# Kernel tuning notes

Hardware: AMD Instinct MI355X
Metric: run time of the kernel (lower is better)

The kernel has to match this reference:

```python
import jax, jax.numpy as jnp
import numpy as np

B, S, D, H = 2, 2048, 2048, 16
HD = D // H            # 128
HALF = HD // 2         # 64
SOFTCAP = 50.0
ROPE_BASE = 10000.0


def setup_inputs() -> dict:
    key = jax.random.key(0)
    k1, k2, k3 = jax.random.split(key, 3)
    inputs = jax.random.normal(k1, (B, S, D), dtype=jnp.float32)
    # param init ~ nnx.initializers.normal() (stddev 0.01 default; scale to keep activations sane)
    w_in = jax.random.normal(k2, (D, H, 3 * HD), dtype=jnp.float32) * (1.0 / np.sqrt(D))
    w_out = jax.random.normal(k3, (H, HD, D), dtype=jnp.float32) * (1.0 / np.sqrt(D))
    # RoPE tables: [S, HALF]
    pos = jnp.arange(S, dtype=jnp.float32)[:, None]
    inv_freq = 1.0 / (ROPE_BASE ** (jnp.arange(HALF, dtype=jnp.float32) / HALF))
    ang = pos * inv_freq[None, :]
    rope_sin = jnp.sin(ang)
    rope_cos = jnp.cos(ang)
    # causal mask [1, 1, S, S]
    mask = jnp.tril(jnp.ones((S, S), dtype=bool))[None, None, :, :]
    return {"inputs": inputs, "w_in": w_in, "w_out": w_out,
            "rope_sin": rope_sin, "rope_cos": rope_cos, "mask": mask}


def apply_rope(x, sin, cos):
    # x: [B, S, H, HD]; sin/cos: [S, HALF] -> broadcast [1, S, 1, HALF]
    sin = sin[None, :, None, :]
    cos = cos[None, :, None, :]
    x1, x2 = x[..., :HALF], x[..., HALF:]
    return jnp.concatenate([x1 * cos - x2 * sin, x2 * cos + x1 * sin], axis=-1)


def reference(inputs, w_in, w_out, rope_sin, rope_cos, mask):
    dtype = inputs.dtype
    # fused QKV projection: [B, S, H, 3*HD]
    qkv = jnp.einsum('bsd,bhf->bshf'.replace('bhf', 'dhf'), inputs, w_in)
    q, k, v = jnp.split(qkv, 3, axis=-1)           # each [B, S, H, HD]
    q = apply_rope(q, rope_sin, rope_cos)
    k = apply_rope(k, rope_sin, rope_cos)
    q = q / jnp.sqrt(jnp.asarray(HD, dtype))
    scores = jnp.einsum('bqhd,bkhd->bhqk', q, k)   # [B, H, S, S]
    big_neg = jnp.finfo(dtype).min
    scores = jnp.where(mask, scores, big_neg)
    scores = jnp.tanh(scores / SOFTCAP) * SOFTCAP  # softcap
    attn = jax.nn.softmax(scores, axis=-1)
    x = jnp.einsum('bhqk,bkhd->bqhd', attn, v)     # [B, S, H, HD]
    out = jnp.einsum('bqhd,hdm->bqm', x, w_out)    # [B, S, D]
    return out
```

## Files before the change

kernel.cpp:

```cpp
#include <hip/hip_runtime.h>

#define B_ 2
#define S_ 2048
#define D_ 2048
#define H_ 16
#define HD_ 128
#define NT_ (S_ / 64)

typedef unsigned short u16;
typedef __bf16 bf16x8 __attribute__((ext_vector_type(8)));
typedef float f32x4 __attribute__((ext_vector_type(4)));
typedef u16 u16x8 __attribute__((ext_vector_type(8)));

__device__ __forceinline__ float bf2f(u16 u) {
  unsigned int x = ((unsigned int)u) << 16;
  return __builtin_bit_cast(float, x);
}
__device__ __forceinline__ u16 f2bf(float f) {
  unsigned int u = __builtin_bit_cast(unsigned int, f);
  u += 0x7fffu + ((u >> 16) & 1u);
  return (u16)(u >> 16);
}
__device__ __forceinline__ void async16(const void* g, void* l) {
  __builtin_amdgcn_global_load_lds((const __attribute__((address_space(1))) void*)g,
                                   (__attribute__((address_space(3))) void*)l, 16, 0, 0);
}
__device__ __forceinline__ float vexp2(float x) {
  float r;
  asm("v_exp_f32 %0, %1" : "=v"(r) : "v"(x));
  return r;
}
__device__ __forceinline__ float vrcp(float x) {
  float r;
  asm("v_rcp_f32 %0, %1" : "=v"(r) : "v"(x));
  return r;
}

__global__ __launch_bounds__(256) void conv_f32_bf16(const float* __restrict__ in,
                                                     u16* __restrict__ outp, int n) {
  int idx = (blockIdx.x * 256 + threadIdx.x) * 4;
  int stride = gridDim.x * 256 * 4;
  for (; idx < n; idx += stride) {
    float4 v = *(const float4*)(in + idx);
    ushort4 ov = make_ushort4(f2bf(v.x), f2bf(v.y), f2bf(v.z), f2bf(v.w));
    *(ushort4*)(outp + idx) = ov;
  }
}

__global__ __launch_bounds__(256) void transpose_win(const float* __restrict__ in,
                                                     u16* __restrict__ outp) {
  __shared__ float tile[32][33];
  int n0 = blockIdx.x * 32, k0 = blockIdx.y * 32;
  int tx = threadIdx.x & 31, ty = threadIdx.x >> 5;
  int n = n0 + tx;
  int cc = n >> 7, p = n & 127;
  int q = (p >> 4) & 3;
  int d = ((p >> 6) << 5) + ((q >> 1) << 4) + ((q & 1) << 6) + (p & 15);
  int f = (cc / 3) * 384 + (cc % 3) * 128 + d;
#pragma unroll
  for (int yy = 0; yy < 32; yy += 8)
    tile[ty + yy][tx] = in[(size_t)(k0 + ty + yy) * 6144 + f];
  __syncthreads();
#pragma unroll
  for (int yy = 0; yy < 32; yy += 8)
    outp[(size_t)(n0 + ty + yy) * 2048 + k0 + tx] = f2bf(tile[tx][ty + yy]);
}

__global__ __launch_bounds__(256) void transpose_wout(const float* __restrict__ in,
                                                      u16* __restrict__ outp) {
  __shared__ float tile[32][33];
  int k0 = blockIdx.x * 32, n0 = blockIdx.y * 32;
  int tx = threadIdx.x & 31, ty = threadIdx.x >> 5;
#pragma unroll
  for (int yy = 0; yy < 32; yy += 8) {
    int kk = k0 + ty + yy;
    int hh = kk >> 7, j = kk & 127;
    int hd = (j & 7) * 16 + (j >> 3);
    tile[ty + yy][tx] = in[(size_t)(hh * 128 + hd) * 2048 + n0 + tx];
  }
  __syncthreads();
#pragma unroll
  for (int yy = 0; yy < 32; yy += 8)
    outp[(size_t)(n0 + ty + yy) * 2048 + k0 + tx] = f2bf(tile[tx][ty + yy]);
}

#define BAR __builtin_amdgcn_s_barrier()
#define LGKM0                                          \
  {                                                    \
    asm volatile("s_waitcnt lgkmcnt(0)" ::: "memory"); \
    __builtin_amdgcn_sched_barrier(0);                 \
  }
#define VM3 asm volatile("s_waitcnt vmcnt(3)" ::: "memory")
#define VM4 asm volatile("s_waitcnt vmcnt(4)" ::: "memory")
#define VM0 asm volatile("s_waitcnt vmcnt(0)" ::: "memory")
#define P1 __builtin_amdgcn_s_setprio(1)
#define P0 __builtin_amdgcn_s_setprio(0)

template <int EPI>
__global__ __launch_bounds__(512, 1) void gemm128(
    const u16* __restrict__ A, const u16* __restrict__ Bt, float* __restrict__ C, int K, int N,
    int ntn, u16* __restrict__ Qo, u16* __restrict__ Ko, u16* __restrict__ Vo,
    const float* __restrict__ rsin, const float* __restrict__ rcos) {
  __shared__ alignas(16) u16 lsA[3][128 * 32];
  __shared__ alignas(16) u16 lsB[3][256 * 32];
  const int tid = threadIdx.x;
  const int lane = tid & 63, wid = tid >> 6;
  const int g = lane >> 4, lr = lane & 15;
  const int wm = wid >> 2, wn = wid & 3;

  const int nwg = ntn << 5;
  const int bid = blockIdx.x;
  const int swz = (bid & 7) * (nwg >> 3) + (bid >> 3);
  const int m_idx = swz & 31, n_idx = swz >> 5;
  const size_t m0 = (size_t)m_idx * 128, n0 = (size_t)n_idx * 256;

  const int rowA = tid >> 2, slA = tid & 3;
  const int rowB0 = tid >> 2;
  const int rowB1 = (512 + tid) >> 2;
  const u16* srcA = A + (m0 + rowA) * K + ((slA ^ ((rowA >> 1) & 3)) << 3);
  const u16* srcB0 = Bt + (n0 + rowB0) * K + ((slA ^ ((rowB0 >> 1) & 3)) << 3);
  const u16* srcB1 = Bt + (n0 + rowB1) * K + ((slA ^ ((rowB1 >> 1) & 3)) << 3);

#define STAGE(t, buf)                                         \
  {                                                           \
    const int koff = (t) << 5;                                \
    async16(srcA + koff, (char*)lsA[buf] + tid * 16);         \
    async16(srcB0 + koff, (char*)lsB[buf] + tid * 16);        \
    async16(srcB1 + koff, (char*)lsB[buf] + 8192 + tid * 16); \
  }

  int ofsA[4], ofsB[4];
#pragma unroll
  for (int i = 0; i < 4; ++i) {
    int ra = wm * 64 + i * 16 + lr;
    ofsA[i] = ra * 64 + ((g ^ ((ra >> 1) & 3)) << 4);
    int rb = wn * 64 + i * 16 + lr;
    ofsB[i] = rb * 64 + ((g ^ ((rb >> 1) & 3)) << 4);
  }

  f32x4 acc[4][4] = {};
  const int nk = K >> 5;

  STAGE(0, 0);
  STAGE(1, 1);
  VM3;
  BAR;

#pragma unroll 1
  for (int kt = 0; kt < nk; ++kt) {
    const int tb = kt % 3;
    const int sb = (kt + 2) % 3;
    bf16x8 aF[4], bF[4];
#pragma unroll
    for (int i = 0; i < 4; ++i) aF[i] = *(const bf16x8*)((const char*)lsA[tb] + ofsA[i]);
#pragma unroll
    for (int j = 0; j < 4; ++j) bF[j] = *(const bf16x8*)((const char*)lsB[tb] + ofsB[j]);
    if (kt + 2 < nk) STAGE(kt + 2, sb);
    BAR;
    LGKM0;
    P1;
#pragma unroll
    for (int i = 0; i < 4; ++i)
#pragma unroll
      for (int j = 0; j < 4; ++j)
        acc[i][j] = __builtin_amdgcn_mfma_f32_16x16x32_bf16(aF[i], bF[j], acc[i][j], 0, 0, 0);
    P0;
    if (kt < nk - 2) {
      VM3;
    } else {
      VM0;
    }
    BAR;
  }
#undef STAGE

  if (EPI == 0) {
#pragma unroll
    for (int i = 0; i < 4; ++i)
#pragma unroll
      for (int j = 0; j < 4; ++j)
#pragma unroll
        for (int r = 0; r < 4; ++r) {
          size_t m = m0 + wm * 64 + i * 16 + 4 * g + r;
          size_t n = n0 + wn * 64 + j * 16 + lr;
          C[m * N + n] = acc[i][j][r];
        }
  } else {
    const int c = (int)(n0 >> 7) + (wn >> 1);
    const int h = c / 3, part = c % 3;
    const int wn1 = wn & 1;
    if (part == 2) {
#pragma unroll
      for (int i = 0; i < 4; ++i) {
        int m = (int)m0 + wm * 64 + i * 16 + 4 * g;
        int b = m >> 11, s = m & (S_ - 1);
#pragma unroll
        for (int j = 0; j < 4; ++j) {
          int hd = wn1 * 32 + ((j >> 1) << 4) + ((j & 1) << 6) + lr;
          ushort4 pk;
          pk.x = f2bf(acc[i][j][0]);
          pk.y = f2bf(acc[i][j][1]);
          pk.z = f2bf(acc[i][j][2]);
          pk.w = f2bf(acc[i][j][3]);
          *(ushort4*)(Vo + ((size_t)(b * H_ + h) * HD_ + hd) * S_ + s) = pk;
        }
      }
    } else {
      u16* dstp = (part == 0) ? Qo : Ko;
      const float scl = (part == 0) ? 0.08838834764831845f : 1.0f;
#pragma unroll
      for (int i = 0; i < 4; ++i) {
        int mbase = (int)m0 + wm * 64 + i * 16 + 4 * g;
#pragma unroll
        for (int r = 0; r < 4; ++r) {
          int m = mbase + r;
          int b = m >> 11, s = m & (S_ - 1);
          const float* srow = rsin + s * 64;
          const float* crow = rcos + s * 64;
          u16* op = dstp + ((size_t)(b * H_ + h) * S_ + s) * HD_ + ((wn1 * 16 + lr) << 2);
          ushort4 pk;
          {
            int d = wn1 * 32 + lr;
            float cv = crow[d] * scl, sv = srow[d] * scl;
            float x1 = acc[i][0][r], x2 = acc[i][1][r];
            pk.x = f2bf(x1 * cv - x2 * sv);
            pk.y = f2bf(x2 * cv + x1 * sv);
          }
          {
            int d = wn1 * 32 + 16 + lr;
            float cv = crow[d] * scl, sv = srow[d] * scl;
            float x1 = acc[i][2][r], x2 = acc[i][3][r];
            pk.z = f2bf(x1 * cv - x2 * sv);
            pk.w = f2bf(x2 * cv + x1 * sv);
          }
          *(ushort4*)op = pk;
        }
      }
    }
  }
}

__global__ __launch_bounds__(256) void attn_fwd(const u16* __restrict__ Q, const u16* __restrict__ K,
                                                const u16* __restrict__ VT, u16* __restrict__ X) {
  const int bh = blockIdx.x;
  const int bx = blockIdx.y;
  const int tid = threadIdx.x;
  const int lane = tid & 63, wid = tid >> 6;
  const int g = lane >> 4, lr = lane & 15;

  __shared__ alignas(16) u16 lsK[2][64 * 128];
  __shared__ alignas(16) u16 lsV[2][128 * 64];
  __shared__ alignas(16) u16 lsP[4][16 * 72];

  const u16* Qp = Q + (size_t)bh * S_ * HD_;
  const u16* Kp = K + (size_t)bh * S_ * HD_;
  const u16* Vp = VT + (size_t)bh * HD_ * S_;
  u16* myP = lsP[wid];
  const int b = bh >> 4, h = bh & 15;

  const float c1 = -0.057707802f;
  const float c2 = -144.26950409f;

#define STG_K(t, bufi)                                                  \
  {                                                                     \
    _Pragma("unroll") for (int p = 0; p < 4; ++p) {                     \
      int c = p * 256 + tid;                                            \
      int rowk = c >> 4;                                                \
      int wsk = ((c & 15) << 4) ^ ((rowk & 7) << 4);                    \
      async16((const char*)Kp + (((size_t)((t)*64 + rowk)) << 8) + wsk, \
              (char*)lsK[bufi] + c * 16);                               \
    }                                                                   \
  }
#define STG_V(t, bufi)                                                   \
  {                                                                      \
    _Pragma("unroll") for (int p = 0; p < 4; ++p) {                      \
      int c = p * 256 + tid;                                             \
      int rowv = c >> 3;                                                 \
      int wsv = ((c & 7) << 4) ^ ((rowv & 7) << 4);                      \
      async16((const char*)Vp + (size_t)rowv * (S_ * 2) + (t)*128 + wsv, \
              (char*)lsV[bufi] + c * 16);                                \
    }                                                                    \
  }

#pragma unroll 1
  for (int pass = 0; pass < 2; ++pass) {
    const int qt = pass ? bx : (NT_ - 1 - bx);
    const int qq = qt * 64 + wid * 16 + lr;

    bf16x8 qf[4];
#pragma unroll
    for (int kc = 0; kc < 4; ++kc)
      qf[kc] = *(const bf16x8*)(Qp + (size_t)qq * HD_ + kc * 32 + g * 8);

    f32x4 o[8] = {};
    float psum = 0.f;

    STG_K(0, 0);
    STG_V(0, 0);
    VM0;
    BAR;

    int cur = 0;
    for (int kt = 0; kt <= qt; ++kt) {
      if (kt < qt) STG_K(kt + 1, cur ^ 1);
      f32x4 sc[4];
#pragma unroll
      for (int jn = 0; jn < 4; ++jn) {
        f32x4 a = {0.f, 0.f, 0.f, 0.f};
        const int row = jn * 16 + lr;
        const int sw = (row & 7) << 4;
#pragma unroll
        for (int kc = 0; kc < 4; ++kc) {
          int w = (kc * 64 + g * 16) ^ sw;
          bf16x8 kf = *(const bf16x8*)((const char*)lsK[cur] + row * 256 + w);
          a = __builtin_amdgcn_mfma_f32_16x16x32_bf16(kf, qf[kc], a, 0, 0, 0);
        }
        sc[jn] = a;
      }
#pragma unroll
      for (int jn = 0; jn < 4; ++jn) {
        const int kbase = kt * 64 + jn * 16 + 4 * g;
        float pv[4];
#pragma unroll
        for (int r = 0; r < 4; ++r) {
          float z = vexp2(c1 * sc[jn][r]);
          float p = vexp2(c2 * z * vrcp(1.f + z));
          if (kbase + r > qq) p = 0.f;
          psum += p;
          pv[r] = p;
        }
        unsigned int w0 = (unsigned int)f2bf(pv[0]) | ((unsigned int)f2bf(pv[1]) << 16);
        unsigned int w1 = (unsigned int)f2bf(pv[2]) | ((unsigned int)f2bf(pv[3]) << 16);
        *(uint2*)(myP + lr * 72 + jn * 16 + 4 * g) = make_uint2(w0, w1);
      }
      if (kt < qt) {
        STG_V(kt + 1, cur ^ 1);
        VM4;
      } else {
        VM0;
      }
      BAR;
#pragma unroll
      for (int kc = 0; kc < 2; ++kc) {
        bf16x8 pa = *(const bf16x8*)(myP + lr * 72 + kc * 32 + g * 8);
#pragma unroll
        for (int jh = 0; jh < 8; ++jh) {
          int row = jh * 16 + lr;
          int w = (kc * 64 + g * 16) ^ ((row & 7) << 4);
          bf16x8 vf = *(const bf16x8*)((const char*)lsV[cur] + row * 128 + w);
          o[jh] = __builtin_amdgcn_mfma_f32_16x16x32_bf16(pa, vf, o[jh], 0, 0, 0);
        }
      }
      BAR;
      cur ^= 1;
    }
    float s = psum;
    s += __shfl_xor(s, 16, 64);
    s += __shfl_xor(s, 32, 64);
    const int qbo = qt * 64 + wid * 16 + 4 * g;
#pragma unroll
    for (int r = 0; r < 4; ++r) {
      float ls = __shfl(s, (lane & 48) | (4 * g + r), 64);
      float inv = 1.f / ls;
      int sq = qbo + r;
      u16x8 pk;
#pragma unroll
      for (int jh = 0; jh < 8; ++jh) pk[jh] = f2bf(o[jh][r] * inv);
      *(u16x8*)(X + ((size_t)(b * S_ + sq)) * D_ + h * HD_ + lr * 8) = pk;
    }
    VM0;
    BAR;
  }
#undef STG_K
#undef STG_V
}

extern "C" void kernel_launch(void* const* d_in, const int* in_sizes, int n_in,
                              void* d_out, int out_size, void* d_ws, size_t ws_size,
                              hipStream_t stream) {
  const float* inputs = (const float*)d_in[0];
  const float* w_in = (const float*)d_in[1];
  const float* w_out = (const float*)d_in[2];
  const float* rsin = (const float*)d_in[3];
  const float* rcos = (const float*)d_in[4];
  float* out = (float*)d_out;

  char* ws = (char*)d_ws;
  u16* bfA = (u16*)(ws);
  u16* w_inT = (u16*)(ws + 16777216);
  u16* Qraw = (u16*)(ws + 41943040);
  u16* Kraw = (u16*)(ws + 58720256);
  u16* VT = (u16*)(ws + 75497472);
  u16* Xbuf = (u16*)(ws);
  u16* w_outT = (u16*)(ws + 16777216);

  conv_f32_bf16<<<2048, 256, 0, stream>>>(inputs, bfA, B_ * S_ * D_);
  transpose_win<<<dim3(192, 64), 256, 0, stream>>>(w_in, w_inT);
  gemm128<1><<<768, 512, 0, stream>>>(bfA, w_inT, nullptr, 2048, 6144, 24, Qraw, Kraw, VT,
                                      rsin, rcos);
  transpose_wout<<<dim3(64, 64), 256, 0, stream>>>(w_out, w_outT);
  attn_fwd<<<dim3(32, NT_ / 2), 256, 0, stream>>>(Qraw, Kraw, VT, Xbuf);
  gemm128<0><<<256, 512, 0, stream>>>(Xbuf, w_outT, out, 2048, 2048, 8,
                                      nullptr, nullptr, nullptr, nullptr, nullptr);
}
```

Before: 271.5 us.

## Merge preprocessing kernels and use 128x128-tile output GEMM with more blocks

Folds the input conversion and both weight transposes into a single prep launch, moving w_outT to its own workspace region so it can be written early. Replaces the 128x256-tile output projection with a dedicated 128x128-tile GEMM launched on 512 blocks instead of 256, which gives better CU occupancy on a 256-CU device. This removes two launches and gap time, but the smaller tiles mean more operand reloads per output.

```diff
diff --git a/kernel.cpp b/kernel.cpp
--- a/kernel.cpp
+++ b/kernel.cpp
@@ -36,52 +36,57 @@
   return r;
 }
 
-__global__ __launch_bounds__(256) void conv_f32_bf16(const float* __restrict__ in,
-                                                     u16* __restrict__ outp, int n) {
-  int idx = (blockIdx.x * 256 + threadIdx.x) * 4;
-  int stride = gridDim.x * 256 * 4;
-  for (; idx < n; idx += stride) {
-    float4 v = *(const float4*)(in + idx);
-    ushort4 ov = make_ushort4(f2bf(v.x), f2bf(v.y), f2bf(v.z), f2bf(v.w));
-    *(ushort4*)(outp + idx) = ov;
-  }
-}
-
-__global__ __launch_bounds__(256) void transpose_win(const float* __restrict__ in,
-                                                     u16* __restrict__ outp) {
+__global__ __launch_bounds__(256) void prep(const float* __restrict__ inputs,
+                                            u16* __restrict__ bfA,
+                                            const float* __restrict__ w_in,
+                                            u16* __restrict__ w_inT,
+                                            const float* __restrict__ w_out,
+                                            u16* __restrict__ w_outT) {
+  const int bid = blockIdx.x;
+  const int tid = threadIdx.x;
+  if (bid < 2048) {
+    const int n = B_ * S_ * D_;
+    int idx = (bid * 256 + tid) * 4;
+    const int stride = 2048 * 256 * 4;
+    for (; idx < n; idx += stride) {
+      float4 v = *(const float4*)(inputs + idx);
+      ushort4 ov = make_ushort4(f2bf(v.x), f2bf(v.y), f2bf(v.z), f2bf(v.w));
+      *(ushort4*)(bfA + idx) = ov;
+    }
+    return;
+  }
   __shared__ float tile[32][33];
-  int n0 = blockIdx.x * 32, k0 = blockIdx.y * 32;
-  int tx = threadIdx.x & 31, ty = threadIdx.x >> 5;
-  int n = n0 + tx;
-  int cc = n >> 7, p = n & 127;
-  int q = (p >> 4) & 3;
-  int d = ((p >> 6) << 5) + ((q >> 1) << 4) + ((q & 1) << 6) + (p & 15);
-  int f = (cc / 3) * 384 + (cc % 3) * 128 + d;
-#pragma unroll
-  for (int yy = 0; yy < 32; yy += 8)
-    tile[ty + yy][tx] = in[(size_t)(k0 + ty + yy) * 6144 + f];
-  __syncthreads();
-#pragma unroll
-  for (int yy = 0; yy < 32; yy += 8)
-    outp[(size_t)(n0 + ty + yy) * 2048 + k0 + tx] = f2bf(tile[tx][ty + yy]);
-}
-
-__global__ __launch_bounds__(256) void transpose_wout(const float* __restrict__ in,
-                                                      u16* __restrict__ outp) {
-  __shared__ float tile[32][33];
-  int k0 = blockIdx.x * 32, n0 = blockIdx.y * 32;
-  int tx = threadIdx.x & 31, ty = threadIdx.x >> 5;
-#pragma unroll
-  for (int yy = 0; yy < 32; yy += 8) {
-    int kk = k0 + ty + yy;
-    int hh = kk >> 7, j = kk & 127;
-    int hd = (j & 7) * 16 + (j >> 3);
-    tile[ty + yy][tx] = in[(size_t)(hh * 128 + hd) * 2048 + n0 + tx];
-  }
-  __syncthreads();
-#pragma unroll
-  for (int yy = 0; yy < 32; yy += 8)
-    outp[(size_t)(n0 + ty + yy) * 2048 + k0 + tx] = f2bf(tile[tx][ty + yy]);
+  int tx = tid & 31, ty = tid >> 5;
+  if (bid < 14336) {
+    const int bb = bid - 2048;
+    const int n0 = (bb % 192) * 32, k0 = (bb / 192) * 32;
+    int n = n0 + tx;
+    int cc = n >> 7, p = n & 127;
+    int q = (p >> 4) & 3;
+    int d = ((p >> 6) << 5) + ((q >> 1) << 4) + ((q & 1) << 6) + (p & 15);
+    int f = (cc / 3) * 384 + (cc % 3) * 128 + d;
+#pragma unroll
+    for (int yy = 0; yy < 32; yy += 8)
+      tile[ty + yy][tx] = w_in[(size_t)(k0 + ty + yy) * 6144 + f];
+    __syncthreads();
+#pragma unroll
+    for (int yy = 0; yy < 32; yy += 8)
+      w_inT[(size_t)(n0 + ty + yy) * 2048 + k0 + tx] = f2bf(tile[tx][ty + yy]);
+  } else {
+    const int bb = bid - 14336;
+    const int k0 = (bb % 64) * 32, n0 = (bb / 64) * 32;
+#pragma unroll
+    for (int yy = 0; yy < 32; yy += 8) {
+      int kk = k0 + ty + yy;
+      int hh = kk >> 7, j = kk & 127;
+      int hd = (j & 7) * 16 + (j >> 3);
+      tile[ty + yy][tx] = w_out[(size_t)(hh * 128 + hd) * 2048 + n0 + tx];
+    }
+    __syncthreads();
+#pragma unroll
+    for (int yy = 0; yy < 32; yy += 8)
+      w_outT[(size_t)(n0 + ty + yy) * 2048 + k0 + tx] = f2bf(tile[tx][ty + yy]);
+  }
 }
 
 #define BAR __builtin_amdgcn_s_barrier()
@@ -90,6 +95,7 @@
     asm volatile("s_waitcnt lgkmcnt(0)" ::: "memory"); \
     __builtin_amdgcn_sched_barrier(0);                 \
   }
+#define VM2 asm volatile("s_waitcnt vmcnt(2)" ::: "memory")
 #define VM3 asm volatile("s_waitcnt vmcnt(3)" ::: "memory")
 #define VM4 asm volatile("s_waitcnt vmcnt(4)" ::: "memory")
 #define VM0 asm volatile("s_waitcnt vmcnt(0)" ::: "memory")
@@ -240,6 +246,94 @@
   }
 }
 
+__global__ __launch_bounds__(512, 1) void gemm_out(const u16* __restrict__ A,
+                                                   const u16* __restrict__ Bt,
+                                                   float* __restrict__ C, int K, int N) {
+  __shared__ alignas(16) u16 lsA[3][128 * 32];
+  __shared__ alignas(16) u16 lsB[3][128 * 32];
+  const int tid = threadIdx.x;
+  const int lane = tid & 63, wid = tid >> 6;
+  const int g = lane >> 4, lr = lane & 15;
+  const int wm = wid >> 1, wn = wid & 1;
+
+  const int nwg = 512;
+  const int bid = blockIdx.x;
+  const int swz = (bid & 7) * (nwg >> 3) + (bid >> 3);
+  const int m_idx = swz & 31, n_idx = swz >> 5;
+  const size_t m0 = (size_t)m_idx * 128, n0 = (size_t)n_idx * 128;
+
+  const int rowq = tid >> 2, slq = tid & 3;
+  const int kofs = (slq ^ ((rowq >> 1) & 3)) << 3;
+  const u16* srcA = A + (m0 + rowq) * K + kofs;
+  const u16* srcB = Bt + (n0 + rowq) * K + kofs;
+
+#define STAGE2(t, buf)                                \
+  {                                                   \
+    const int koff = (t) << 5;                        \
+    async16(srcA + koff, (char*)lsA[buf] + tid * 16); \
+    async16(srcB + koff, (char*)lsB[buf] + tid * 16); \
+  }
+
+  int ofsA[2], ofsB[4];
+#pragma unroll
+  for (int i = 0; i < 2; ++i) {
+    int ra = wm * 32 + i * 16 + lr;
+    ofsA[i] = ra * 64 + ((g ^ ((ra >> 1) & 3)) << 4);
+  }
+#pragma unroll
+  for (int j = 0; j < 4; ++j) {
+    int rb = wn * 64 + j * 16 + lr;
+    ofsB[j] = rb * 64 + ((g ^ ((rb >> 1) & 3)) << 4);
+  }
+
+  f32x4 acc[2][4] = {};
+  const int nk = K >> 5;
+
+  STAGE2(0, 0);
+  STAGE2(1, 1);
+  VM2;
+  BAR;
+
+#pragma unroll 1
+  for (int kt = 0; kt < nk; ++kt) {
+    const int tb = kt % 3;
+    const int sb = (kt + 2) % 3;
+    bf16x8 aF[2], bF[4];
+#pragma unroll
+    for (int i = 0; i < 2; ++i) aF[i] = *(const bf16x8*)((const char*)lsA[tb] + ofsA[i]);
+#pragma unroll
+    for (int j = 0; j < 4; ++j) bF[j] = *(const bf16x8*)((const char*)lsB[tb] + ofsB[j]);
+    if (kt + 2 < nk) STAGE2(kt + 2, sb);
+    BAR;
+    LGKM0;
+    P1;
+#pragma unroll
+    for (int i = 0; i < 2; ++i)
+#pragma unroll
+      for (int j = 0; j < 4; ++j)
+        acc[i][j] = __builtin_amdgcn_mfma_f32_16x16x32_bf16(aF[i], bF[j], acc[i][j], 0, 0, 0);
+    P0;
+    if (kt < nk - 2) {
+      VM2;
+    } else {
+      VM0;
+    }
+    BAR;
+  }
+#undef STAGE2
+
+#pragma unroll
+  for (int i = 0; i < 2; ++i)
+#pragma unroll
+    for (int j = 0; j < 4; ++j)
+#pragma unroll
+      for (int r = 0; r < 4; ++r) {
+        size_t m = m0 + wm * 32 + i * 16 + 4 * g + r;
+        size_t n = n0 + wn * 64 + j * 16 + lr;
+        C[m * N + n] = acc[i][j][r];
+      }
+}
+
 __global__ __launch_bounds__(256) void attn_fwd(const u16* __restrict__ Q, const u16* __restrict__ K,
                                                 const u16* __restrict__ VT, u16* __restrict__ X) {
   const int bh = blockIdx.x;
@@ -391,15 +485,12 @@
   u16* Qraw = (u16*)(ws + 41943040);
   u16* Kraw = (u16*)(ws + 58720256);
   u16* VT = (u16*)(ws + 75497472);
+  u16* w_outT = (u16*)(ws + 92274688);
   u16* Xbuf = (u16*)(ws);
-  u16* w_outT = (u16*)(ws + 16777216);
-
-  conv_f32_bf16<<<2048, 256, 0, stream>>>(inputs, bfA, B_ * S_ * D_);
-  transpose_win<<<dim3(192, 64), 256, 0, stream>>>(w_in, w_inT);
+
+  prep<<<18432, 256, 0, stream>>>(inputs, bfA, w_in, w_inT, w_out, w_outT);
   gemm128<1><<<768, 512, 0, stream>>>(bfA, w_inT, nullptr, 2048, 6144, 24, Qraw, Kraw, VT,
                                       rsin, rcos);
-  transpose_wout<<<dim3(64, 64), 256, 0, stream>>>(w_out, w_outT);
   attn_fwd<<<dim3(32, NT_ / 2), 256, 0, stream>>>(Qraw, Kraw, VT, Xbuf);
-  gemm128<0><<<256, 512, 0, stream>>>(Xbuf, w_outT, out, 2048, 2048, 8,
-                                      nullptr, nullptr, nullptr, nullptr, nullptr);
-}
+  gemm_out<<<512, 512, 0, stream>>>(Xbuf, w_outT, out, 2048, 2048);
+}
```

Result: faster. 263.9 us (-2.8%).
